# Kernel tuning notes

Hardware: AMD Instinct MI355X
Metric: run time of the kernel (lower is better)

The kernel has to match this reference:

```python
import jax, jax.numpy as jnp
import numpy as np

N_NODES = 100000
N_EDGES = 1600000
IN_FEATS, HID_FEATS, OUT_FEATS = 64, 64, 32


def setup_inputs() -> dict:
    key = jax.random.key(0)
    ks = jax.random.split(key, 8)
    x = jax.random.normal(ks[0], (N_NODES, IN_FEATS), dtype=jnp.float32)
    edge_index = jax.random.randint(ks[1], (2, N_EDGES), 0, N_NODES, dtype=jnp.int64)
    s1 = 1.0 / np.sqrt(IN_FEATS)
    s2 = 1.0 / np.sqrt(HID_FEATS)
    return {
        "x": x,
        "edge_index": edge_index,
        "W1l": jax.random.uniform(ks[2], (IN_FEATS, HID_FEATS), jnp.float32, -s1, s1),
        "W1r": jax.random.uniform(ks[3], (IN_FEATS, HID_FEATS), jnp.float32, -s1, s1),
        "b1": jnp.zeros((HID_FEATS,), jnp.float32),
        "W2l": jax.random.uniform(ks[4], (HID_FEATS, OUT_FEATS), jnp.float32, -s2, s2),
        "W2r": jax.random.uniform(ks[5], (HID_FEATS, OUT_FEATS), jnp.float32, -s2, s2),
        "b2": jnp.zeros((OUT_FEATS,), jnp.float32),
    }


def _mean_aggregate(h, src, dst, n_nodes):
    # gather source features, scatter-mean into destination nodes
    msg_sum = jax.ops.segment_sum(h[src], dst, num_segments=n_nodes)  # [N, D]
    cnt = jax.ops.segment_sum(jnp.ones(src.shape, h.dtype), dst, num_segments=n_nodes)
    return msg_sum / jnp.maximum(cnt, 1.0)[:, None]  # zero in-degree -> 0


def _sage_conv(h, src, dst, Wl, Wr, b):
    # PyG SAGEConv: lin_l(mean_j x_j) + lin_r(x_i); bias lives in lin_l
    agg = _mean_aggregate(h, src, dst, h.shape[0])
    return agg @ Wl + h @ Wr + b


def reference(x, edge_index, W1l, W1r, b1, W2l, W2r, b2):
    src, dst = edge_index[0], edge_index[1]
    h = jax.nn.relu(_sage_conv(x, src, dst, W1l, W1r, b1))
    out = _sage_conv(h, src, dst, W2l, W2r, b2)
    return out
```

## Files before the change

### kernel.cpp

```cpp
#include <hip/hip_runtime.h>

#define NN 100000
#define NE 1600000
#define NBK 196
#define CAPB 12288
#define CVTB 6250

typedef __attribute__((ext_vector_type(8))) short bf16x8;
typedef __attribute__((ext_vector_type(4))) float f32x4;

__device__ __forceinline__ unsigned short f2b(float f) {
  unsigned b = __float_as_uint(f);
  unsigned r = b + 0x7FFF + ((b >> 16) & 1);
  return (unsigned short)(r >> 16);
}

__global__ void k_pre(const float* __restrict__ x, unsigned short* __restrict__ xb,
                      const float* __restrict__ W1l, const float* __restrict__ W1r,
                      unsigned short* __restrict__ WT1,
                      const float* __restrict__ W2l, const float* __restrict__ W2r,
                      unsigned short* __restrict__ WT2,
                      const int* __restrict__ src, const int* __restrict__ dst,
                      int* __restrict__ gcur, unsigned* __restrict__ pairbuf) {
  __shared__ int hist[NBK], base[NBK], lofs[NBK];
  int t = threadIdx.x;
  int b = blockIdx.x;
  if (b < CVTB) {
    int i = (b * 256 + t) * 4;
    float4 v = *(const float4*)(x + i);
    ushort4 o;
    o.x = f2b(v.x); o.y = f2b(v.y); o.z = f2b(v.z); o.w = f2b(v.w);
    *(ushort4*)(xb + i) = o;
    return;
  }
  if (b == CVTB) {
    for (int i = t; i < 64 * 128; i += 256) {
      int f = i >> 7, k = i & 127;
      WT1[i] = f2b((k < 64) ? W1l[k * 64 + f] : W1r[(k - 64) * 64 + f]);
    }
    return;
  }
  if (b == CVTB + 1) {
    for (int i = t; i < 32 * 128; i += 256) {
      int f = i >> 7, k = i & 127;
      WT2[i] = f2b((k < 64) ? W2l[k * 32 + f] : W2r[(k - 64) * 32 + f]);
    }
    return;
  }
  int pb = b - (CVTB + 2);
  for (int i = t; i < NBK; i += 256) hist[i] = 0;
  __syncthreads();
  unsigned pk[16]; int bk[16];
  int e0 = pb * 4096 + t;
#pragma unroll
  for (int j = 0; j < 16; ++j) {
    int e = e0 + j * 256;
    if (e < NE) {
      int d = dst[e], s = src[e];
      bk[j] = d >> 9;
      pk[j] = ((unsigned)s << 9) | (unsigned)(d & 511);
      atomicAdd(&hist[bk[j]], 1);
    } else bk[j] = -1;
  }
  __syncthreads();
  for (int i = t; i < NBK; i += 256) {
    base[i] = atomicAdd(&gcur[i], hist[i]);
    lofs[i] = 0;
  }
  __syncthreads();
#pragma unroll
  for (int j = 0; j < 16; ++j) {
    if (bk[j] >= 0) {
      int lp = base[bk[j]] + atomicAdd(&lofs[bk[j]], 1);
      if (lp < CAPB) pairbuf[(size_t)bk[j] * CAPB + lp] = pk[j];
    }
  }
}

__global__ void k_partB(const unsigned* __restrict__ pairbuf, const int* __restrict__ gcur,
                        int* __restrict__ esrc, uint2* __restrict__ rowp2) {
  __shared__ int cnt[512], cur[512], ssum[512];
  __shared__ int ebuf[CAPB];
  int b = blockIdx.x, t = threadIdx.x;
  int cb = gcur[b]; if (cb > CAPB) cb = CAPB;
  cnt[t] = 0;
  __syncthreads();
  const unsigned* pb = pairbuf + (size_t)b * CAPB;
  for (int i = t; i < cb; i += 512) atomicAdd(&cnt[pb[i] & 511], 1);
  __syncthreads();
  int a0 = cnt[t];
  ssum[t] = a0;
  __syncthreads();
  for (int off = 1; off < 512; off <<= 1) {
    int tmp = (t >= off) ? ssum[t - off] : 0;
    __syncthreads();
    ssum[t] += tmp;
    __syncthreads();
  }
  int ex = ssum[t] - a0;
  cur[t] = ex;
  __syncthreads();
  int n = b * 512 + t;
  if (n < NN) rowp2[n] = make_uint2((unsigned)(b * CAPB + ex),
                                    (unsigned)(b * CAPB + ex + a0));
  for (int i = t; i < cb; i += 512) {
    unsigned p = pb[i];
    int pos = atomicAdd(&cur[p & 511], 1);
    ebuf[pos] = (int)(p >> 9);
  }
  __syncthreads();
  for (int i = t; i < cb; i += 512) esrc[(size_t)b * CAPB + i] = ebuf[i];
}

__global__ void k_agg(const uint2* __restrict__ fb64, const uint2* __restrict__ rowp2,
                      const int* __restrict__ esrc, uint2* __restrict__ aggb64) {
  int tid = blockIdx.x * 256 + threadIdx.x;
  int node = tid >> 4;
  int c16 = tid & 15;
  int qbase = (threadIdx.x & 63) & 48;
  uint2 rp = rowp2[node];
  int beg = (int)rp.x, deg = (int)(rp.y - rp.x);
  float a0 = 0.f, a1 = 0.f, a2 = 0.f, a3 = 0.f;

  for (int r0 = 0; r0 < deg; r0 += 16) {
    int rem = deg - r0; if (rem > 16) rem = 16;
    int idxv = esrc[beg + r0 + (c16 < rem ? c16 : 0)];
#pragma unroll 8
    for (int j = 0; j < rem; ++j) {
      int s = __shfl(idxv, qbase + j);
      uint2 v = fb64[(size_t)s * 16 + c16];
      a0 += __uint_as_float(v.x << 16);
      a1 += __uint_as_float(v.x & 0xFFFF0000u);
      a2 += __uint_as_float(v.y << 16);
      a3 += __uint_as_float(v.y & 0xFFFF0000u);
    }
  }
  float inv = (deg > 0) ? (1.0f / (float)deg) : 0.f;
  uint2 o;
  o.x = (unsigned)f2b(a0 * inv) | ((unsigned)f2b(a1 * inv) << 16);
  o.y = (unsigned)f2b(a2 * inv) | ((unsigned)f2b(a3 * inv) << 16);
  aggb64[(size_t)node * 16 + c16] = o;
}

template <int NF>
__global__ __launch_bounds__(256) void k_gemm(
    const unsigned short* __restrict__ aggb, const unsigned short* __restrict__ featb,
    const unsigned short* __restrict__ WT, const float* __restrict__ bias,
    float* __restrict__ out, unsigned short* __restrict__ ob, int relu) {
  __shared__ unsigned short As[64 * 128];
  __shared__ unsigned short Ws[NF * 128];
  int tid = threadIdx.x;
  int n0 = blockIdx.x * 64;
  int lane = tid & 63, wr = tid >> 6;

  for (int cch = tid; cch < 64 * 16; cch += 256) {
    int r = cch >> 4, s = cch & 15;
    int n = n0 + r;
    bf16x8 v = {0, 0, 0, 0, 0, 0, 0, 0};
    if (n < NN) {
      const unsigned short* p = (s < 8) ? (aggb + (size_t)n * 64 + s * 8)
                                        : (featb + (size_t)n * 64 + (s - 8) * 8);
      v = *(const bf16x8*)p;
    }
    *(bf16x8*)(&As[r * 128 + ((s ^ (r & 15)) << 3)]) = v;
  }
  for (int cch = tid; cch < NF * 16; cch += 256) {
    int f = cch >> 4, s = cch & 15;
    bf16x8 v = *(const bf16x8*)(WT + f * 128 + s * 8);
    *(bf16x8*)(&Ws[f * 128 + ((s ^ (f & 15)) << 3)]) = v;
  }
  __syncthreads();

  int l15 = lane & 15, lg = lane >> 4;
  int arow = wr * 16 + l15;
  f32x4 acc[NF / 16];
#pragma unroll
  for (int ct = 0; ct < NF / 16; ++ct) acc[ct] = (f32x4){0.f, 0.f, 0.f, 0.f};

#pragma unroll
  for (int k0 = 0; k0 < 4; ++k0) {
    int sa = k0 * 4 + lg;
    bf16x8 a = *(const bf16x8*)(&As[arow * 128 + ((sa ^ (arow & 15)) << 3)]);
#pragma unroll
    for (int ct = 0; ct < NF / 16; ++ct) {
      int bcol = ct * 16 + l15;
      bf16x8 b = *(const bf16x8*)(&Ws[bcol * 128 + ((sa ^ (bcol & 15)) << 3)]);
      acc[ct] = __builtin_amdgcn_mfma_f32_16x16x32_bf16(a, b, acc[ct], 0, 0, 0);
    }
  }

#pragma unroll
  for (int ct = 0; ct < NF / 16; ++ct) {
    int f = ct * 16 + l15;
    float bv = bias[f];
#pragma unroll
    for (int r = 0; r < 4; ++r) {
      int n = n0 + wr * 16 + lg * 4 + r;
      if (n >= NN) continue;
      float v = acc[ct][r] + bv;
      if (relu) v = fmaxf(v, 0.f);
      if (out) out[(size_t)n * NF + f] = v;
      if (ob) ob[(size_t)n * NF + f] = f2b(v);
    }
  }
}

extern "C" void kernel_launch(void* const* d_in, const int* in_sizes, int n_in,
                              void* d_out, int out_size, void* d_ws, size_t ws_size,
                              hipStream_t stream) {
  const float* x   = (const float*)d_in[0];
  const int*   ei  = (const int*)d_in[1];
  const float* W1l = (const float*)d_in[2];
  const float* W1r = (const float*)d_in[3];
  const float* b1  = (const float*)d_in[4];
  const float* W2l = (const float*)d_in[5];
  const float* W2r = (const float*)d_in[6];
  const float* b2  = (const float*)d_in[7];
  const int* src = ei;
  const int* dst = ei + NE;
  float* out = (float*)d_out;

  char* ws = (char*)d_ws;
  size_t off = 0;
  auto take = [&](size_t bytes) -> char* {
    char* p = ws + off;
    off = (off + bytes + 255) & ~(size_t)255;
    return p;
  };
  int*      gcur    = (int*)take((size_t)NBK * 4);
  unsigned* pairbuf = (unsigned*)take((size_t)NBK * CAPB * 4);
  int*      esrc    = (int*)take((size_t)NBK * CAPB * 4);
  uint2*    rowp2   = (uint2*)take((size_t)NN * 8);
  unsigned short* aggb = (unsigned short*)take((size_t)NN * 64 * 2);
  unsigned short* xb   = (unsigned short*)take((size_t)NN * 64 * 2);
  unsigned short* hb   = (unsigned short*)take((size_t)NN * 64 * 2);
  unsigned short* WT1  = (unsigned short*)take((size_t)64 * 128 * 2);
  unsigned short* WT2  = (unsigned short*)take((size_t)32 * 128 * 2);

  hipMemsetAsync(gcur, 0, (size_t)NBK * 4, stream);

  int nbA = (NE + 4095) / 4096;
  k_pre<<<CVTB + 2 + nbA, 256, 0, stream>>>(x, xb, W1l, W1r, WT1, W2l, W2r, WT2,
                                            src, dst, gcur, pairbuf);
  k_partB<<<NBK, 512, 0, stream>>>(pairbuf, gcur, esrc, rowp2);

  int nbG = (NN + 63) / 64;
  k_agg<<<NN / 16, 256, 0, stream>>>((const uint2*)xb, rowp2, esrc, (uint2*)aggb);
  k_gemm<64><<<nbG, 256, 0, stream>>>(aggb, xb, WT1, b1, nullptr, hb, 1);
  k_agg<<<NN / 16, 256, 0, stream>>>((const uint2*)hb, rowp2, esrc, (uint2*)aggb);
  k_gemm<32><<<nbG, 256, 0, stream>>>(aggb, hb, WT2, b2, out, nullptr, 0);
}
```

Measured before the change: 158.2 us.

## Split bf16 feature tables into 16-column slabs and aggregate per slab

```diff
diff --git a/kernel.cpp b/kernel.cpp
--- a/kernel.cpp
+++ b/kernel.cpp
@@ -5,6 +5,7 @@
 #define NBK 196
 #define CAPB 12288
 #define CVTB 6250
+#define SLAB (NN * 16)
 
 typedef __attribute__((ext_vector_type(8))) short bf16x8;
 typedef __attribute__((ext_vector_type(4))) float f32x4;
@@ -13,6 +14,10 @@
   unsigned b = __float_as_uint(f);
   unsigned r = b + 0x7FFF + ((b >> 16) & 1);
   return (unsigned short)(r >> 16);
+}
+
+__global__ void k_zero(int* __restrict__ g) {
+  if (threadIdx.x < NBK) g[threadIdx.x] = 0;
 }
 
 __global__ void k_pre(const float* __restrict__ x, unsigned short* __restrict__ xb,
@@ -27,10 +32,11 @@
   int b = blockIdx.x;
   if (b < CVTB) {
     int i = (b * 256 + t) * 4;
+    int n = i >> 6, f = i & 63;
     float4 v = *(const float4*)(x + i);
     ushort4 o;
     o.x = f2b(v.x); o.y = f2b(v.y); o.z = f2b(v.z); o.w = f2b(v.w);
-    *(ushort4*)(xb + i) = o;
+    *(ushort4*)(xb + (size_t)(f >> 4) * SLAB + (size_t)n * 16 + (f & 15)) = o;
     return;
   }
   if (b == CVTB) {
@@ -112,34 +118,29 @@
   for (int i = t; i < cb; i += 512) esrc[(size_t)b * CAPB + i] = ebuf[i];
 }
 
-__global__ void k_agg(const uint2* __restrict__ fb64, const uint2* __restrict__ rowp2,
-                      const int* __restrict__ esrc, uint2* __restrict__ aggb64) {
+__global__ void k_agg(const unsigned* __restrict__ slab_u, const uint2* __restrict__ rowp2,
+                      const int* __restrict__ esrc, unsigned* __restrict__ out_u) {
   int tid = blockIdx.x * 256 + threadIdx.x;
-  int node = tid >> 4;
-  int c16 = tid & 15;
-  int qbase = (threadIdx.x & 63) & 48;
+  int node = tid >> 3;
+  int c8 = tid & 7;
+  int gbase = (threadIdx.x & 63) & 56;
   uint2 rp = rowp2[node];
   int beg = (int)rp.x, deg = (int)(rp.y - rp.x);
-  float a0 = 0.f, a1 = 0.f, a2 = 0.f, a3 = 0.f;
-
-  for (int r0 = 0; r0 < deg; r0 += 16) {
-    int rem = deg - r0; if (rem > 16) rem = 16;
-    int idxv = esrc[beg + r0 + (c16 < rem ? c16 : 0)];
+  float a0 = 0.f, a1 = 0.f;
+  for (int r0 = 0; r0 < deg; r0 += 8) {
+    int rem = deg - r0; if (rem > 8) rem = 8;
+    int idxv = esrc[beg + r0 + (c8 < rem ? c8 : 0)];
 #pragma unroll 8
     for (int j = 0; j < rem; ++j) {
-      int s = __shfl(idxv, qbase + j);
-      uint2 v = fb64[(size_t)s * 16 + c16];
-      a0 += __uint_as_float(v.x << 16);
-      a1 += __uint_as_float(v.x & 0xFFFF0000u);
-      a2 += __uint_as_float(v.y << 16);
-      a3 += __uint_as_float(v.y & 0xFFFF0000u);
+      int s = __shfl(idxv, gbase + j);
+      unsigned v = slab_u[(size_t)s * 8 + c8];
+      a0 += __uint_as_float(v << 16);
+      a1 += __uint_as_float(v & 0xFFFF0000u);
     }
   }
   float inv = (deg > 0) ? (1.0f / (float)deg) : 0.f;
-  uint2 o;
-  o.x = (unsigned)f2b(a0 * inv) | ((unsigned)f2b(a1 * inv) << 16);
-  o.y = (unsigned)f2b(a2 * inv) | ((unsigned)f2b(a3 * inv) << 16);
-  aggb64[(size_t)node * 16 + c16] = o;
+  out_u[(size_t)node * 8 + c8] =
+      (unsigned)f2b(a0 * inv) | ((unsigned)f2b(a1 * inv) << 16);
 }
 
 template <int NF>
@@ -158,9 +159,10 @@
     int n = n0 + r;
     bf16x8 v = {0, 0, 0, 0, 0, 0, 0, 0};
     if (n < NN) {
-      const unsigned short* p = (s < 8) ? (aggb + (size_t)n * 64 + s * 8)
-                                        : (featb + (size_t)n * 64 + (s - 8) * 8);
-      v = *(const bf16x8*)p;
+      const unsigned short* basep = (s < 8) ? aggb : featb;
+      int ss = s & 7;
+      v = *(const bf16x8*)(basep + (size_t)(ss >> 1) * SLAB + (size_t)n * 16 +
+                           (ss & 1) * 8);
     }
     *(bf16x8*)(&As[r * 128 + ((s ^ (r & 15)) << 3)]) = v;
   }
@@ -200,7 +202,7 @@
       float v = acc[ct][r] + bv;
       if (relu) v = fmaxf(v, 0.f);
       if (out) out[(size_t)n * NF + f] = v;
-      if (ob) ob[(size_t)n * NF + f] = f2b(v);
+      if (ob) ob[(size_t)ct * SLAB + (size_t)n * 16 + l15] = f2b(v);
     }
   }
 }
@@ -237,16 +239,22 @@
   unsigned short* WT1  = (unsigned short*)take((size_t)64 * 128 * 2);
   unsigned short* WT2  = (unsigned short*)take((size_t)32 * 128 * 2);
 
-  hipMemsetAsync(gcur, 0, (size_t)NBK * 4, stream);
-
   int nbA = (NE + 4095) / 4096;
+  k_zero<<<1, 256, 0, stream>>>(gcur);
   k_pre<<<CVTB + 2 + nbA, 256, 0, stream>>>(x, xb, W1l, W1r, WT1, W2l, W2r, WT2,
                                             src, dst, gcur, pairbuf);
   k_partB<<<NBK, 512, 0, stream>>>(pairbuf, gcur, esrc, rowp2);
 
   int nbG = (NN + 63) / 64;
-  k_agg<<<NN / 16, 256, 0, stream>>>((const uint2*)xb, rowp2, esrc, (uint2*)aggb);
+  int nbAgg = NN / 32;
+  for (int p = 0; p < 4; ++p)
+    k_agg<<<nbAgg, 256, 0, stream>>>((const unsigned*)xb + (size_t)p * (SLAB / 2),
+                                     rowp2, esrc,
+                                     (unsigned*)aggb + (size_t)p * (SLAB / 2));
   k_gemm<64><<<nbG, 256, 0, stream>>>(aggb, xb, WT1, b1, nullptr, hb, 1);
-  k_agg<<<NN / 16, 256, 0, stream>>>((const uint2*)hb, rowp2, esrc, (uint2*)aggb);
+  for (int p = 0; p < 4; ++p)
+    k_agg<<<nbAgg, 256, 0, stream>>>((const unsigned*)hb + (size_t)p * (SLAB / 2),
+                                     rowp2, esrc,
+                                     (unsigned*)aggb + (size_t)p * (SLAB / 2));
   k_gemm<32><<<nbG, 256, 0, stream>>>(aggb, hb, WT2, b2, out, nullptr, 0);
 }
```

Measured after the change: 238.1 us. 50.6% more time.
